# Optimization experiments

Measured on AMD Instinct MI355X. Metric: run time of the kernel, lower is better.

The kernel has to match this reference:

```python
import jax, jax.numpy as jnp
import numpy as np

H = 256       # hiddenDim
E = 300       # embDim
VOCAB = 50000
S = 1024      # number of sentences in document
L = 64        # words per sentence (chain-tree depth)
TOPIC = 100
TARGET = 5


def setup_inputs() -> dict:
    key = jax.random.key(0)
    ks = jax.random.split(key, 21)
    f32 = jnp.float32
    return {
        'sentenceInIndex': jax.random.randint(ks[0], (S, L), 0, VOCAB),
        'depTypes': jax.random.randint(ks[1], (S, L - 1), 0, 9),
        'D_T_distr': jax.random.uniform(ks[2], (TOPIC,), dtype=f32),
        'h0': jax.random.normal(ks[3], (H,), dtype=f32),
        'idx2vec': jax.random.normal(ks[4], (VOCAB, E), dtype=f32) * 0.1,
        'q': jax.random.normal(ks[5], (10, H), dtype=f32) * 0.1,
        'W': jax.random.normal(ks[6], (3 * H, E), dtype=f32) * 0.05,
        'U': jax.random.normal(ks[7], (3 * H, H), dtype=f32) * 0.05,
        'D': jax.random.normal(ks[8], (3 * H, H), dtype=f32) * 0.05,
        'b': jax.random.normal(ks[9], (3 * H,), dtype=f32) * 0.05,
        'gru_wih': jax.random.normal(ks[10], (3 * H, H), dtype=f32) * 0.05,
        'gru_whh': jax.random.normal(ks[11], (3 * H, H), dtype=f32) * 0.05,
        'gru_bih': jax.random.normal(ks[12], (3 * H,), dtype=f32) * 0.05,
        'gru_bhh': jax.random.normal(ks[13], (3 * H,), dtype=f32) * 0.05,
        'gate_W': jax.random.normal(ks[14], (2 * H, H), dtype=f32) * 0.05,
        'gate_U': jax.random.normal(ks[15], (2 * H, H), dtype=f32) * 0.05,
        'gate_b': jax.random.normal(ks[16], (2 * H,), dtype=f32) * 0.05,
        'mlp_W': jax.random.normal(ks[17], (H, TOPIC), dtype=f32) * 0.05,
        'mlp_b': jax.random.normal(ks[18], (H,), dtype=f32) * 0.05,
        'out_W': jax.random.normal(ks[19], (TARGET, H), dtype=f32) * 0.05,
        'out_b': jax.random.normal(ks[20], (TARGET,), dtype=f32) * 0.05,
    }


def reference(sentenceInIndex, depTypes, D_T_distr, h0, idx2vec, q, W, U, D, b,
              gru_wih, gru_whh, gru_bih, gru_bhh,
              gate_W, gate_U, gate_b, mlp_W, mlp_b, out_W, out_b):
    # ---- DERNN over chain-canonicalized dependency trees (vectorized over S sentences) ----
    x = idx2vec[sentenceInIndex]                        # [S, L, E] gather
    Wx = jnp.einsum('sle,ke->slk', x, W)                # [S, L, 3H]
    qe = q[depTypes]                                    # [S, L-1, H] dep-type embeddings for edges k->k+1
    Dq = jnp.einsum('slh,kh->slk', qe, D)               # [S, L-1, 3H]

    # leaf node (position L-1): q_sum = q[-1] ('leafNotion'); no child h term
    dq_leaf = D @ q[-1]                                 # [3H]
    iu_leaf = Wx[:, -1, H:] + dq_leaf[H:] + b[H:]       # [S, 2H]
    h = jnp.tanh(jax.nn.sigmoid(iu_leaf[:, :H]) * jnp.tanh(iu_leaf[:, H:]))  # [S, H]

    # internal nodes k = L-2 .. 0, single child k+1 (edge k)
    pre = Wx[:, :L - 1] + Dq + b                        # [S, L-1, 3H]
    pre_rev = jnp.swapaxes(pre[:, ::-1], 0, 1)          # [L-1, S, 3H] bottom-up order

    def tree_step(h_c, pre_k):
        tot = pre_k + h_c @ U.T                         # [S, 3H]
        f = jax.nn.sigmoid(tot[:, :H]) * h_c            # child forget gate * child h (single child => sum)
        i = jax.nn.sigmoid(tot[:, H:2 * H])
        u = jnp.tanh(tot[:, 2 * H:])
        h_n = jnp.tanh(i * u + f)
        return h_n, None

    sentenceVector, _ = jax.lax.scan(tree_step, h, pre_rev)  # [S, H] root hidden per sentence

    # ---- GRU over sentence sequence (batch 1), torch nn.GRU math ----
    def gru_step(hh, xt):
        gi = gru_wih @ xt + gru_bih                     # [3H]
        gh = gru_whh @ hh + gru_bhh
        r = jax.nn.sigmoid(gi[:H] + gh[:H])
        z = jax.nn.sigmoid(gi[H:2 * H] + gh[H:2 * H])
        n = jnp.tanh(gi[2 * H:] + r * gh[2 * H:])
        return (1.0 - z) * n + z * hh, None

    hT, _ = jax.lax.scan(gru_step, h0, sentenceVector)  # [H] final hidden state

    # ---- topic vector, GATE fusion, classifier ----
    t = jnp.tanh(mlp_W @ D_T_distr + mlp_b)             # [H]
    g = gate_W @ hT + gate_U @ t + gate_b               # [2H]
    v = jnp.tanh(jax.nn.sigmoid(g[:H]) * hT + jax.nn.sigmoid(g[H:]) * t)
    return jax.nn.softmax(out_W @ v + out_b)            # [TARGET]
```

## Files before the change

kernel.cpp:

```cpp
#include <hip/hip_runtime.h>

typedef short short8 __attribute__((ext_vector_type(8)));
typedef float f4 __attribute__((ext_vector_type(4)));
typedef int i4 __attribute__((ext_vector_type(4)));
typedef _Float16 half8 __attribute__((ext_vector_type(8)));
typedef _Float16 h2 __attribute__((ext_vector_type(2)));

#define HD 256
#define ED 300
#define EP 320
#define TH 768
#define NS 1024
#define LW 64
#define SH 4.5f

#define BAR_LDS() do { asm volatile("s_waitcnt lgkmcnt(0)" ::: "memory"); \
                       __builtin_amdgcn_s_barrier(); } while (0)

__device__ __forceinline__ unsigned short f2bf(float f) {
    unsigned int u = __float_as_uint(f);
    u = (u + 0x7FFFu + ((u >> 16) & 1u)) >> 16;
    return (unsigned short)u;
}
__device__ __forceinline__ float bf2f(unsigned short s) {
    return __uint_as_float(((unsigned int)s) << 16);
}
__device__ __forceinline__ float sigm(float x) {
    return __builtin_amdgcn_rcpf(1.f + __expf(-x));
}
__device__ __forceinline__ float tanh_(float x) {
    x = fminf(fmaxf(x, -15.f), 15.f);
    return 1.f - 2.f * __builtin_amdgcn_rcpf(1.f + __expf(2.f * x));
}
__device__ __forceinline__ unsigned int pack_h2(float a, float b) {
    h2 p; p.x = (_Float16)a; p.y = (_Float16)b;
    return __builtin_bit_cast(unsigned int, p);
}

__device__ __forceinline__ void load8bf(const unsigned short* p, float* o) {
    uint4 a = *(const uint4*)p;
    o[0] = bf2f((unsigned short)(a.x & 0xffff)); o[1] = bf2f((unsigned short)(a.x >> 16));
    o[2] = bf2f((unsigned short)(a.y & 0xffff)); o[3] = bf2f((unsigned short)(a.y >> 16));
    o[4] = bf2f((unsigned short)(a.z & 0xffff)); o[5] = bf2f((unsigned short)(a.z >> 16));
    o[6] = bf2f((unsigned short)(a.w & 0xffff)); o[7] = bf2f((unsigned short)(a.w >> 16));
}
__device__ __forceinline__ void ubf4(uint2 a, float* o) {
    o[0] = bf2f((unsigned short)(a.x & 0xffff)); o[1] = bf2f((unsigned short)(a.x >> 16));
    o[2] = bf2f((unsigned short)(a.y & 0xffff)); o[3] = bf2f((unsigned short)(a.y >> 16));
}

__global__ void k_prep(const float* __restrict__ W, const float* __restrict__ U,
                       const float* __restrict__ Wih, const float* __restrict__ Whh,
                       const float* __restrict__ q, const float* __restrict__ Dm,
                       const float* __restrict__ DT, const float* __restrict__ mlpW,
                       const float* __restrict__ mlpb,
                       const float* __restrict__ bih, const float* __restrict__ bhh,
                       unsigned short* __restrict__ Wb, _Float16* __restrict__ Uh,
                       _Float16* __restrict__ Wihh,
                       signed char* __restrict__ Wq, float* __restrict__ rowscale,
                       float* __restrict__ bias2,
                       float* __restrict__ Dq, float* __restrict__ tv) {
    __shared__ float smax[4];
    int bid = blockIdx.x, tid = threadIdx.x;
    if (bid < 768) {
        int r = bid;
        for (int j = tid; j < EP; j += 256)
            Wb[r * EP + j] = (j < ED) ? f2bf(W[r * ED + j]) : (unsigned short)0;
        float whv = Whh[r * HD + tid];
        for (int j = tid; j < HD; j += 256) {
            Uh[r * HD + j] = (_Float16)U[r * HD + j];
            Wihh[r * HD + j] = (_Float16)Wih[r * HD + j];
        }
        float v = fabsf(whv);
        for (int o = 32; o; o >>= 1) v = fmaxf(v, __shfl_xor(v, o));
        if ((tid & 63) == 0) smax[tid >> 6] = v;
        __syncthreads();
        float am = fmaxf(fmaxf(smax[0], smax[1]), fmaxf(smax[2], smax[3]));
        float inv = (am > 0.f) ? 127.f / am : 0.f;
        int qi = (int)rintf(whv * inv);
        qi = max(-127, min(127, qi));
        Wq[r * HD + tid] = (signed char)qi;
        if (tid == 0) rowscale[r] = (am / 127.f) * (SH / 127.f);
    } else if (bid < 798) {
        int idx = bid - 768;
        int d = idx / 3, part = idx - d * 3;
        int n = part * 256 + tid;
        float s = 0.f;
        for (int h = 0; h < HD; ++h) s += Dm[n * HD + h] * q[d * HD + h];
        Dq[d * TH + n] = s;
    } else {
        if (tid < HD) {
            float s = 0.f;
            for (int k = 0; k < 100; ++k) s += mlpW[tid * 100 + k] * DT[k];
            tv[tid] = tanh_(s + mlpb[tid]);
        }
        for (int r = tid; r < TH; r += 256)
            bias2[r] = bih[r] + ((r < 512) ? bhh[r] : 0.f);
    }
}

#define XP 328
__launch_bounds__(256, 2)
__global__ void k_phaseB(const int* __restrict__ sIdx, const int* __restrict__ depT,
                         const float* __restrict__ emb, const unsigned short* __restrict__ Wb,
                         const float* __restrict__ Dq, const float* __restrict__ bias,
                         unsigned short* __restrict__ pre) {
    __shared__ float dq_s[10 * 772];
    __shared__ float b_s[TH];
    __shared__ int dep_s[32];
    __shared__ int idx_s[32];
    __shared__ __align__(16) unsigned short xbf[32 * XP];
    __shared__ __align__(16) unsigned short tbuf[16 * 776];
    int tid = threadIdx.x;
    int c0 = blockIdx.x * 32;
    for (int i = tid; i < 10 * 768; i += 256) {
        int d = i / 768, n = i - d * 768;
        dq_s[d * 772 + n] = Dq[i];
    }
    for (int i = tid; i < TH; i += 256) b_s[i] = bias[i];
    if (tid < 32) {
        int m = c0 + tid;
        idx_s[tid] = sIdx[m];
        int l = m & 63, s = m >> 6;
        dep_s[tid] = (l == 63) ? 9 : depT[s * 63 + l];
    }
    __syncthreads();
    for (int i = tid; i < 32 * EP; i += 256) {
        int row = i / EP, col = i - row * EP;
        unsigned short v = 0;
        if (col < ED) v = f2bf(emb[(long)idx_s[row] * ED + col]);
        xbf[row * XP + col] = v;
    }
    __syncthreads();

    int lane = tid & 63;
    int w = tid >> 6;
    int quad = lane >> 4, l16 = lane & 15;

    f4 acc[2][12];
#pragma unroll
    for (int cs = 0; cs < 2; ++cs)
#pragma unroll
        for (int ms = 0; ms < 12; ++ms) acc[cs][ms] = (f4){0.f, 0.f, 0.f, 0.f};

    const unsigned short* wbase = Wb + (w * 192 + l16) * EP;

#pragma unroll
    for (int kt = 0; kt < 10; ++kt) {
        int k0 = kt * 32 + quad * 8;
        short8 bf0 = *(const short8*)&xbf[l16 * XP + k0];
        short8 bf1 = *(const short8*)&xbf[(16 + l16) * XP + k0];
#pragma unroll
        for (int ms = 0; ms < 12; ++ms) {
            short8 af = *(const short8*)(wbase + ms * 16 * EP + k0);
            acc[0][ms] = __builtin_amdgcn_mfma_f32_16x16x32_bf16(af, bf0, acc[0][ms], 0, 0, 0);
            acc[1][ms] = __builtin_amdgcn_mfma_f32_16x16x32_bf16(af, bf1, acc[1][ms], 0, 0, 0);
        }
    }

#pragma unroll
    for (int cs = 0; cs < 2; ++cs) {
        int dep = dep_s[cs * 16 + l16];
#pragma unroll
        for (int ms = 0; ms < 12; ++ms) {
            int ncol = w * 192 + ms * 16 + quad * 4;
            f4 dq4 = *(const f4*)&dq_s[dep * 772 + ncol];
            f4 b4 = *(const f4*)&b_s[ncol];
            unsigned int lo = (unsigned int)f2bf(acc[cs][ms][0] + dq4[0] + b4[0]) |
                              ((unsigned int)f2bf(acc[cs][ms][1] + dq4[1] + b4[1]) << 16);
            unsigned int hi = (unsigned int)f2bf(acc[cs][ms][2] + dq4[2] + b4[2]) |
                              ((unsigned int)f2bf(acc[cs][ms][3] + dq4[3] + b4[3]) << 16);
            uint2 v; v.x = lo; v.y = hi;
            *(uint2*)&tbuf[l16 * 776 + ncol] = v;
        }
        __syncthreads();
        for (int it = 0; it < 6; ++it) {
            int flat = it * 256 + tid;
            int row = flat / 96;
            int ch = flat - row * 96;
            uint4 v = *(const uint4*)&tbuf[row * 776 + ch * 8];
            *(uint4*)(pre + (long)(c0 + cs * 16 + row) * TH + ch * 8) = v;
        }
        __syncthreads();
    }
}

#define NSB 4
__global__ void __launch_bounds__(768) k_phaseC(
                         const unsigned short* __restrict__ pre,
                         const _Float16* __restrict__ Uh,
                         const _Float16* __restrict__ Wihh,
                         const float* __restrict__ bias2,
                         float* __restrict__ gi) {
    __shared__ __align__(16) uint4 hfr[512];
    __shared__ __align__(16) float tot[16 * 772];
    int tid = threadIdx.x;
    int lane = tid & 63, w = tid >> 6, quad = lane >> 4, l16 = lane & 15;
    int s0 = blockIdx.x * NSB;

    uint4 frag[32];
    {
        const _Float16* base = Uh + (w * 64 + l16) * HD;
#pragma unroll
        for (int t = 0; t < 4; ++t)
#pragma unroll
            for (int kt = 0; kt < 8; ++kt)
                frag[t * 8 + kt] = *(const uint4*)(base + t * 16 * HD + kt * 32 + quad * 8);
    }

    int us = tid >> 5;
    int jg = tid & 31;
    int j0 = jg * 8;
    int hcell = (j0 >> 5) * 64 + 16 * ((j0 >> 3) & 3) + us;
    uint4 hcp;
    bool act = (tid < 512);
    bool real = act && (us < NSB);

    if (act) {
        if (real) {
            const unsigned short* prow = pre + ((long)(s0 + us) * LW + 63) * TH;
            float iv[8], uv[8], hcv[8];
            load8bf(prow + 256 + j0, iv);
            load8bf(prow + 512 + j0, uv);
#pragma unroll
            for (int r = 0; r < 8; ++r) hcv[r] = tanh_(sigm(iv[r]) * tanh_(uv[r]));
            hcp.x = pack_h2(hcv[0], hcv[1]); hcp.y = pack_h2(hcv[2], hcv[3]);
            hcp.z = pack_h2(hcv[4], hcv[5]); hcp.w = pack_h2(hcv[6], hcv[7]);
        } else {
            hcp.x = 0u; hcp.y = 0u; hcp.z = 0u; hcp.w = 0u;
        }
        hfr[hcell] = hcp;
    }
    __syncthreads();

    int mb = w * 64 + quad * 4;

    for (int step = 0; step < 63; ++step) {
        int l = 62 - step;
        uint2 praw[6];
        if (real) {
            const unsigned short* prow = pre + ((long)(s0 + us) * LW + l) * TH;
#pragma unroll
            for (int g = 0; g < 3; ++g) {
                praw[2 * g]     = *(const uint2*)(prow + g * 256 + j0);
                praw[2 * g + 1] = *(const uint2*)(prow + g * 256 + j0 + 4);
            }
        }
        f4 a0 = (f4){0,0,0,0}, a1 = (f4){0,0,0,0}, a2 = (f4){0,0,0,0}, a3 = (f4){0,0,0,0};
#pragma unroll
        for (int kt = 0; kt < 8; ++kt) {
            half8 b = __builtin_bit_cast(half8, hfr[kt * 64 + lane]);
            a0 = __builtin_amdgcn_mfma_f32_16x16x32_f16(__builtin_bit_cast(half8, frag[kt]), b, a0, 0, 0, 0);
            a1 = __builtin_amdgcn_mfma_f32_16x16x32_f16(__builtin_bit_cast(half8, frag[8 + kt]), b, a1, 0, 0, 0);
            a2 = __builtin_amdgcn_mfma_f32_16x16x32_f16(__builtin_bit_cast(half8, frag[16 + kt]), b, a2, 0, 0, 0);
            a3 = __builtin_amdgcn_mfma_f32_16x16x32_f16(__builtin_bit_cast(half8, frag[24 + kt]), b, a3, 0, 0, 0);
        }
        float* tr = tot + l16 * 772;
        *(f4*)&tr[mb] = a0;
        *(f4*)&tr[mb + 16] = a1;
        *(f4*)&tr[mb + 32] = a2;
        *(f4*)&tr[mb + 48] = a3;
        BAR_LDS();
        if (real) {
            const float* ts = tot + us * 772;
            float hcv[8];
            h2 px = __builtin_bit_cast(h2, hcp.x); h2 py = __builtin_bit_cast(h2, hcp.y);
            h2 pz = __builtin_bit_cast(h2, hcp.z); h2 pw = __builtin_bit_cast(h2, hcp.w);
            hcv[0] = (float)px.x; hcv[1] = (float)px.y; hcv[2] = (float)py.x; hcv[3] = (float)py.y;
            hcv[4] = (float)pz.x; hcv[5] = (float)pz.y; hcv[6] = (float)pw.x; hcv[7] = (float)pw.y;
#pragma unroll
            for (int hf = 0; hf < 2; ++hf) {
                int jb = j0 + hf * 4;
                float pf[4], pi_[4], pu[4];
                ubf4(praw[hf], pf);
                ubf4(praw[2 + hf], pi_);
                ubf4(praw[4 + hf], pu);
                f4 tf = *(const f4*)&ts[jb];
                f4 ti = *(const f4*)&ts[256 + jb];
                f4 tu = *(const f4*)&ts[512 + jb];
#pragma unroll
                for (int r = 0; r < 4; ++r) {
                    float ff = tf[r] + pf[r];
                    float ii = ti[r] + pi_[r];
                    float uu = tu[r] + pu[r];
                    hcv[hf * 4 + r] = tanh_(sigm(ii) * tanh_(uu) + sigm(ff) * hcv[hf * 4 + r]);
                }
            }
            hcp.x = pack_h2(hcv[0], hcv[1]); hcp.y = pack_h2(hcv[2], hcv[3]);
            hcp.z = pack_h2(hcv[4], hcv[5]); hcp.w = pack_h2(hcv[6], hcv[7]);
            hfr[hcell] = hcp;
        }
        BAR_LDS();
    }

    {
        const _Float16* base = Wihh + (w * 64 + l16) * HD;
#pragma unroll
        for (int t = 0; t < 4; ++t)
#pragma unroll
            for (int kt = 0; kt < 8; ++kt)
                frag[t * 8 + kt] = *(const uint4*)(base + t * 16 * HD + kt * 32 + quad * 8);
    }
    f4 a0 = (f4){0,0,0,0}, a1 = (f4){0,0,0,0}, a2 = (f4){0,0,0,0}, a3 = (f4){0,0,0,0};
#pragma unroll
    for (int kt = 0; kt < 8; ++kt) {
        half8 b = __builtin_bit_cast(half8, hfr[kt * 64 + lane]);
        a0 = __builtin_amdgcn_mfma_f32_16x16x32_f16(__builtin_bit_cast(half8, frag[kt]), b, a0, 0, 0, 0);
        a1 = __builtin_amdgcn_mfma_f32_16x16x32_f16(__builtin_bit_cast(half8, frag[8 + kt]), b, a1, 0, 0, 0);
        a2 = __builtin_amdgcn_mfma_f32_16x16x32_f16(__builtin_bit_cast(half8, frag[16 + kt]), b, a2, 0, 0, 0);
        a3 = __builtin_amdgcn_mfma_f32_16x16x32_f16(__builtin_bit_cast(half8, frag[24 + kt]), b, a3, 0, 0, 0);
    }
    if (l16 < NSB) {
        float* go = gi + (long)(s0 + l16) * TH;
        f4 b0 = *(const f4*)(bias2 + mb);
        f4 b1 = *(const f4*)(bias2 + mb + 16);
        f4 b2 = *(const f4*)(bias2 + mb + 32);
        f4 b3 = *(const f4*)(bias2 + mb + 48);
        *(f4*)(go + mb) = a0 + b0;
        *(f4*)(go + mb + 16) = a1 + b1;
        *(f4*)(go + mb + 32) = a2 + b2;
        *(f4*)(go + mb + 48) = a3 + b3;
    }
}

#define GB 8
__global__ void __launch_bounds__(512) k_gru(
                      const signed char* __restrict__ Wq, const float* __restrict__ rowscale,
                      const float* __restrict__ bhh,
                      const float* __restrict__ gi, const float* __restrict__ h0,
                      const float* __restrict__ tv,
                      const float* __restrict__ gateW, const float* __restrict__ gateU,
                      const float* __restrict__ gateb,
                      const float* __restrict__ outW, const float* __restrict__ outb,
                      float* __restrict__ out,
                      float* __restrict__ hstate, int t0, int do_head) {
    __shared__ __align__(16) signed char qbuf[2][HD];
    __shared__ __align__(16) float gbuf[2][GB * TH];
    __shared__ float hts[HD];
    __shared__ float sgs[512];
    __shared__ float vvs[HD];
    __shared__ float lg[8];

    int tid = threadIdx.x;
    int lane = tid & 63, w = tid >> 6, quad = lane >> 4, l16 = lane & 15;

    i4 far_[2][4], faz[2][4], fan[2][4];
#pragma unroll
    for (int c = 0; c < 2; ++c) {
        const signed char* qr_ = Wq + (long)(w * 32 + c * 16 + l16) * HD;
        const signed char* qz_ = Wq + (long)(256 + w * 32 + c * 16 + l16) * HD;
        const signed char* qn_ = Wq + (long)(512 + w * 32 + c * 16 + l16) * HD;
#pragma unroll
        for (int kc = 0; kc < 4; ++kc) {
            far_[c][kc] = *(const i4*)(qr_ + kc * 64 + quad * 16);
            faz[c][kc] = *(const i4*)(qz_ + kc * 64 + quad * 16);
            fan[c][kc] = *(const i4*)(qn_ + kc * 64 + quad * 16);
        }
    }

    int sc = (l16 >> 2) & 1;
    int sr = l16 & 3;
    int j = w * 32 + sc * 16 + quad * 4 + sr;
    bool b2 = (sr & 2) != 0, b1 = (sr & 1) != 0, bc = (sc != 0);
    bool owner = (l16 < 8);

    float rs_r = rowscale[j];
    float rs_z = rowscale[256 + j];
    float rs_n = rowscale[512 + j];
    float bn_l = bhh[512 + j];

    float hv = (t0 == 0) ? h0[j] : hstate[j];
    if (owner) {
        float hc = fminf(fmaxf(hv, -SH), SH);
        qbuf[0][j] = (signed char)(int)rintf(hc * (127.f / SH));
    }
    const int nb0 = t0 / GB;
    float rg[12];
    {
        const float* g0 = gi + (long)nb0 * GB * TH;
        const float* g1 = gi + (long)(nb0 + 1) * GB * TH;
#pragma unroll
        for (int i = 0; i < 12; ++i) gbuf[0][i * 512 + tid] = g0[i * 512 + tid];
#pragma unroll
        for (int i = 0; i < 12; ++i) rg[i] = g1[i * 512 + tid];
    }
    __syncthreads();

    for (int nbr = 0; nbr < 256 / GB; ++nbr) {
        int nb = nb0 + nbr;
        int buf = nbr & 1;
#pragma unroll
        for (int u = 0; u < GB; ++u) {
            if (u == 0) {
#pragma unroll
                for (int i = 0; i < 12; ++i) gbuf[buf ^ 1][i * 512 + tid] = rg[i];
                if (nb + 2 < NS / GB) {
                    const float* gsrc = gi + (long)(nb + 2) * GB * TH;
#pragma unroll
                    for (int i = 0; i < 12; ++i) rg[i] = gsrc[i * 512 + tid];
                }
            }
            const int p = u & 1;
            const float* gl = &gbuf[buf][u * TH];
            float gr_l = gl[j], gz_l = gl[256 + j], gn_l = gl[512 + j];

            i4 qr[2], qz[2], qn[2];
#pragma unroll
            for (int c = 0; c < 2; ++c) { qr[c] = (i4){0,0,0,0}; qz[c] = (i4){0,0,0,0}; qn[c] = (i4){0,0,0,0}; }
#pragma unroll
            for (int kc = 0; kc < 4; ++kc) {
                i4 b = *(const i4*)&qbuf[p][kc * 64 + quad * 16];
                qr[0] = __builtin_amdgcn_mfma_i32_16x16x64_i8(far_[0][kc], b, qr[0], 0, 0, 0);
                qr[1] = __builtin_amdgcn_mfma_i32_16x16x64_i8(far_[1][kc], b, qr[1], 0, 0, 0);
                qz[0] = __builtin_amdgcn_mfma_i32_16x16x64_i8(faz[0][kc], b, qz[0], 0, 0, 0);
                qz[1] = __builtin_amdgcn_mfma_i32_16x16x64_i8(faz[1][kc], b, qz[1], 0, 0, 0);
                qn[0] = __builtin_amdgcn_mfma_i32_16x16x64_i8(fan[0][kc], b, qn[0], 0, 0, 0);
                qn[1] = __builtin_amdgcn_mfma_i32_16x16x64_i8(fan[1][kc], b, qn[1], 0, 0, 0);
            }
            int ra0 = bc ? qr[1][0] : qr[0][0], ra1 = bc ? qr[1][1] : qr[0][1];
            int ra2 = bc ? qr[1][2] : qr[0][2], ra3 = bc ? qr[1][3] : qr[0][3];
            int rt0 = b2 ? ra2 : ra0, rt1 = b2 ? ra3 : ra1;
            int qrv = b1 ? rt1 : rt0;
            int za0 = bc ? qz[1][0] : qz[0][0], za1 = bc ? qz[1][1] : qz[0][1];
            int za2 = bc ? qz[1][2] : qz[0][2], za3 = bc ? qz[1][3] : qz[0][3];
            int zt0 = b2 ? za2 : za0, zt1 = b2 ? za3 : za1;
            int qzv = b1 ? zt1 : zt0;
            int na0 = bc ? qn[1][0] : qn[0][0], na1 = bc ? qn[1][1] : qn[0][1];
            int na2 = bc ? qn[1][2] : qn[0][2], na3 = bc ? qn[1][3] : qn[0][3];
            int nt0 = b2 ? na2 : na0, nt1 = b2 ? na3 : na1;
            int qnv = b1 ? nt1 : nt0;
            float rv = sigm(gr_l + (float)qrv * rs_r);
            float zv = sigm(gz_l + (float)qzv * rs_z);
            float nv = tanh_(gn_l + rv * ((float)qnv * rs_n + bn_l));
            hv = (1.f - zv) * nv + zv * hv;
            if (owner) {
                float hc = fminf(fmaxf(hv, -SH), SH);
                qbuf[p ^ 1][j] = (signed char)(int)rintf(hc * (127.f / SH));
            }
            __syncthreads();
        }
    }

    if (!do_head) {
        if (owner) hstate[j] = hv;
        return;
    }

    if (owner) hts[j] = hv;
    __syncthreads();
    {
        float s = gateb[tid];
        for (int k = 0; k < HD; ++k)
            s += gateW[tid * HD + k] * hts[k] + gateU[tid * HD + k] * tv[k];
        sgs[tid] = sigm(s);
    }
    __syncthreads();
    if (tid < HD) vvs[tid] = tanh_(sgs[tid] * hts[tid] + sgs[256 + tid] * tv[tid]);
    __syncthreads();
    if (tid < 5) {
        float s = outb[tid];
        for (int k = 0; k < HD; ++k) s += outW[tid * HD + k] * vvs[k];
        lg[tid] = s;
    }
    __syncthreads();
    if (tid == 0) {
        float m = lg[0];
        for (int i = 1; i < 5; ++i) m = fmaxf(m, lg[i]);
        float e[5], sum = 0.f;
        for (int i = 0; i < 5; ++i) { e[i] = __expf(lg[i] - m); sum += e[i]; }
        for (int i = 0; i < 5; ++i) out[i] = e[i] / sum;
    }
}

extern "C" void kernel_launch(void* const* d_in, const int* in_sizes, int n_in,
                              void* d_out, int out_size, void* d_ws, size_t ws_size,
                              hipStream_t stream) {
    (void)in_sizes; (void)n_in; (void)out_size; (void)ws_size;
    const int* sIdx = (const int*)d_in[0];
    const int* depT = (const int*)d_in[1];
    const float* DT = (const float*)d_in[2];
    const float* h0 = (const float*)d_in[3];
    const float* emb = (const float*)d_in[4];
    const float* q = (const float*)d_in[5];
    const float* W = (const float*)d_in[6];
    const float* U = (const float*)d_in[7];
    const float* Dm = (const float*)d_in[8];
    const float* b = (const float*)d_in[9];
    const float* Wih = (const float*)d_in[10];
    const float* Whh = (const float*)d_in[11];
    const float* bih = (const float*)d_in[12];
    const float* bhh = (const float*)d_in[13];
    const float* gateW = (const float*)d_in[14];
    const float* gateU = (const float*)d_in[15];
    const float* gateb = (const float*)d_in[16];
    const float* mlpW = (const float*)d_in[17];
    const float* mlpb = (const float*)d_in[18];
    const float* outW = (const float*)d_in[19];
    const float* outb = (const float*)d_in[20];

    char* ws = (char*)d_ws;
    unsigned short* Wb = (unsigned short*)ws;   ws += 768 * 320 * 2;
    _Float16* Uh = (_Float16*)ws;               ws += 768 * 256 * 2;
    _Float16* Wihh = (_Float16*)ws;             ws += 768 * 256 * 2;
    signed char* Wq = (signed char*)ws;         ws += 768 * 256;
    float* rowscale = (float*)ws;               ws += 768 * 4;
    float* bias2 = (float*)ws;                  ws += 768 * 4;
    float* Dq = (float*)ws;                     ws += 10 * 768 * 4;
    float* tv = (float*)ws;                     ws += 1024;
    float* hstate = (float*)ws;                 ws += 1024;
    ws = (char*)d_ws + ((((size_t)(ws - (char*)d_ws)) + 4095) & ~(size_t)4095);
    unsigned short* pre = (unsigned short*)ws;  ws += (size_t)65536 * 768 * 2;
    float* gi = (float*)ws;                     ws += (size_t)1024 * 768 * 4;

    k_prep<<<dim3(799), dim3(256), 0, stream>>>(W, U, Wih, Whh, q, Dm, DT, mlpW, mlpb,
                                                bih, bhh,
                                                Wb, Uh, Wihh, Wq, rowscale, bias2, Dq, tv);
    k_phaseB<<<dim3(2048), dim3(256), 0, stream>>>(sIdx, depT, emb, Wb, Dq, b, pre);
    k_phaseC<<<dim3(256), dim3(768), 0, stream>>>(pre, Uh, Wihh, bias2, gi);
    k_gru<<<dim3(1), dim3(512), 0, stream>>>(Wq, rowscale, bhh, gi, h0, tv,
                                             gateW, gateU, gateb, outW, outb, (float*)d_out,
                                             hstate, 0, 0);
    k_gru<<<dim3(1), dim3(512), 0, stream>>>(Wq, rowscale, bhh, gi, h0, tv,
                                             gateW, gateU, gateb, outW, outb, (float*)d_out,
                                             hstate, 256, 0);
    k_gru<<<dim3(1), dim3(512), 0, stream>>>(Wq, rowscale, bhh, gi, h0, tv,
                                             gateW, gateU, gateb, outW, outb, (float*)d_out,
                                             hstate, 512, 0);
    k_gru<<<dim3(1), dim3(512), 0, stream>>>(Wq, rowscale, bhh, gi, h0, tv,
                                             gateW, gateU, gateb, outW, outb, (float*)d_out,
                                             hstate, 768, 1);
}
```

Baseline: 1.162 ms.

## Slim phase-B LDS usage, vectorize embedding gather, write outputs directly

Phase B no longer stages the Dq table, bias, indices, dependency types or an output transpose buffer in shared memory. Those values are now read from global memory, which should hit in cache, and results are written straight to the pre buffer as 8-byte stores. The embedding gather now uses float4 loads. With the smaller LDS footprint the launch bound is raised to 4 blocks per CU to improve occupancy. The cost is less coalesced output stores and more global loads in the epilogue.

```diff
diff --git a/kernel.cpp b/kernel.cpp
--- a/kernel.cpp
+++ b/kernel.cpp
@@ -100,36 +100,26 @@
 }
 
 #define XP 328
-__launch_bounds__(256, 2)
+__launch_bounds__(256, 4)
 __global__ void k_phaseB(const int* __restrict__ sIdx, const int* __restrict__ depT,
                          const float* __restrict__ emb, const unsigned short* __restrict__ Wb,
                          const float* __restrict__ Dq, const float* __restrict__ bias,
                          unsigned short* __restrict__ pre) {
-    __shared__ float dq_s[10 * 772];
-    __shared__ float b_s[TH];
-    __shared__ int dep_s[32];
-    __shared__ int idx_s[32];
     __shared__ __align__(16) unsigned short xbf[32 * XP];
-    __shared__ __align__(16) unsigned short tbuf[16 * 776];
     int tid = threadIdx.x;
     int c0 = blockIdx.x * 32;
-    for (int i = tid; i < 10 * 768; i += 256) {
-        int d = i / 768, n = i - d * 768;
-        dq_s[d * 772 + n] = Dq[i];
-    }
-    for (int i = tid; i < TH; i += 256) b_s[i] = bias[i];
-    if (tid < 32) {
-        int m = c0 + tid;
-        idx_s[tid] = sIdx[m];
-        int l = m & 63, s = m >> 6;
-        dep_s[tid] = (l == 63) ? 9 : depT[s * 63 + l];
-    }
-    __syncthreads();
-    for (int i = tid; i < 32 * EP; i += 256) {
-        int row = i / EP, col = i - row * EP;
-        unsigned short v = 0;
-        if (col < ED) v = f2bf(emb[(long)idx_s[row] * ED + col]);
-        xbf[row * XP + col] = v;
+
+    for (int i = tid; i < 32 * 80; i += 256) {
+        int row = i / 80, c4 = i - row * 80;
+        unsigned int lo = 0, hi = 0;
+        if (c4 < 75) {
+            int idx = sIdx[c0 + row];
+            float4 v = *(const float4*)(emb + (long)idx * ED + c4 * 4);
+            lo = (unsigned int)f2bf(v.x) | ((unsigned int)f2bf(v.y) << 16);
+            hi = (unsigned int)f2bf(v.z) | ((unsigned int)f2bf(v.w) << 16);
+        }
+        uint2 pv; pv.x = lo; pv.y = hi;
+        *(uint2*)&xbf[row * XP + c4 * 4] = pv;
     }
     __syncthreads();
 
@@ -160,28 +150,23 @@
 
 #pragma unroll
     for (int cs = 0; cs < 2; ++cs) {
-        int dep = dep_s[cs * 16 + l16];
+        int xr = c0 + cs * 16 + l16;
+        int l = xr & 63, s = xr >> 6;
+        int dep = (l == 63) ? 9 : depT[s * 63 + l];
+        const float* dqrow = Dq + dep * TH;
+        unsigned short* prow = pre + (long)xr * TH;
 #pragma unroll
         for (int ms = 0; ms < 12; ++ms) {
             int ncol = w * 192 + ms * 16 + quad * 4;
-            f4 dq4 = *(const f4*)&dq_s[dep * 772 + ncol];
-            f4 b4 = *(const f4*)&b_s[ncol];
+            f4 dq4 = *(const f4*)&dqrow[ncol];
+            f4 b4 = *(const f4*)&bias[ncol];
             unsigned int lo = (unsigned int)f2bf(acc[cs][ms][0] + dq4[0] + b4[0]) |
                               ((unsigned int)f2bf(acc[cs][ms][1] + dq4[1] + b4[1]) << 16);
             unsigned int hi = (unsigned int)f2bf(acc[cs][ms][2] + dq4[2] + b4[2]) |
                               ((unsigned int)f2bf(acc[cs][ms][3] + dq4[3] + b4[3]) << 16);
             uint2 v; v.x = lo; v.y = hi;
-            *(uint2*)&tbuf[l16 * 776 + ncol] = v;
-        }
-        __syncthreads();
-        for (int it = 0; it < 6; ++it) {
-            int flat = it * 256 + tid;
-            int row = flat / 96;
-            int ch = flat - row * 96;
-            uint4 v = *(const uint4*)&tbuf[row * 776 + ch * 8];
-            *(uint4*)(pre + (long)(c0 + cs * 16 + row) * TH + ch * 8) = v;
-        }
-        __syncthreads();
+            *(uint2*)(prow + ncol) = v;
+        }
     }
 }
 
```

Measured after the change: 1.227 ms. 1.06x slower.
